# Kernel optimization log

Hardware: AMD Instinct MI355X
Metric: run time of the kernel (lower is better)

## Reference

```python
import jax, jax.numpy as jnp
import numpy as np

B, S, D, H = 2, 2048, 2048, 16
HD = D // H  # 128


def _rope_tables(seq_len, head_dim, base=10000.0):
    inv_freq = 1.0 / (base ** (np.arange(0, head_dim, 2, dtype=np.float32) / head_dim))
    t = np.arange(seq_len, dtype=np.float32)
    freqs = np.outer(t, inv_freq)  # [S, HD/2]
    return jnp.asarray(np.cos(freqs)), jnp.asarray(np.sin(freqs))


def setup_inputs() -> dict:
    key = jax.random.key(0)
    ks = jax.random.split(key, 5)
    std = 0.02
    inp = {
        "x": jax.random.normal(ks[0], (B, S, D), jnp.float32),
        "wq": jax.random.normal(ks[1], (D, D), jnp.float32) * std,
        "bq": jnp.zeros((D,), jnp.float32),
        "wk": jax.random.normal(ks[2], (D, D), jnp.float32) * std,
        "bk": jnp.zeros((D,), jnp.float32),
        "wv": jax.random.normal(ks[3], (D, D), jnp.float32) * std,
        "bv": jnp.zeros((D,), jnp.float32),
        "wo": jax.random.normal(ks[4], (D, D), jnp.float32) * std,
        "bo": jnp.zeros((D,), jnp.float32),
    }
    cos, sin = _rope_tables(S, HD)
    inp["freqs_cos"], inp["freqs_sin"] = cos, sin
    return inp


def _apply_rope(t, cos, sin):
    # t: [B,S,H,HD]; cos/sin: [S,HD/2] -> broadcast [1,S,1,HD/2]
    tp = t.reshape(*t.shape[:-1], HD // 2, 2)
    t1, t2 = tp[..., 0], tp[..., 1]
    c = cos[None, :, None, :]
    s = sin[None, :, None, :]
    out = jnp.stack([t1 * c - t2 * s, t1 * s + t2 * c], axis=-1)
    return out.reshape(t.shape)


def reference(x, wq, bq, wk, bk, wv, bv, wo, bo, freqs_cos, freqs_sin):
    b, s, d = x.shape
    q = (x @ wq.T + bq).reshape(b, s, H, HD)
    k = (x @ wk.T + bk).reshape(b, s, H, HD)
    v = (x @ wv.T + bv).reshape(b, s, H, HD)
    q = _apply_rope(q, freqs_cos, freqs_sin)
    k = _apply_rope(k, freqs_cos, freqs_sin)
    # causal SDPA: scores [B,H,S,S]
    scale = 1.0 / jnp.sqrt(jnp.asarray(HD, x.dtype))
    scores = jnp.einsum("bqhd,bkhd->bhqk", q, k) * scale
    causal = jnp.tril(jnp.ones((s, s), bool))
    scores = jnp.where(causal[None, None], scores, jnp.asarray(-1e30, scores.dtype))
    attn = jax.nn.softmax(scores.astype(jnp.float32), axis=-1).astype(x.dtype)
    out = jnp.einsum("bhqk,bkhd->bqhd", attn, v).reshape(b, s, d)
    return out @ wo.T + bo
```

## Files before the change

### kernel.cpp

```cpp
#include <hip/hip_runtime.h>


typedef __attribute__((ext_vector_type(8))) short short8;
typedef __attribute__((ext_vector_type(4))) float f32x4;
typedef __attribute__((ext_vector_type(16))) float f32x16;
typedef __attribute__((ext_vector_type(2))) unsigned short u16x2;
typedef __attribute__((ext_vector_type(4))) unsigned short u16x4;
typedef __attribute__((ext_vector_type(8))) unsigned short u16x8;

constexpr int Bc = 2, Sc = 2048, Dc = 2048, Hc = 16, HDc = 128;
constexpr int Mc = Bc * Sc;
constexpr int Nc = Dc, Kc = Dc;
constexpr int NT = Kc / 64;
constexpr float QSCL = 0.08838834764831845f * 1.4426950408889634f;

__device__ __forceinline__ unsigned short f2bf(float f) {
    union { float f; unsigned u; } x; x.f = f;
    unsigned r = x.u + 0x7FFFu + ((x.u >> 16) & 1u);
    return (unsigned short)(r >> 16);
}
__device__ __forceinline__ float bf2f(unsigned short u) {
    union { float f; unsigned u; } x; x.u = (unsigned)u << 16; return x.f;
}

__device__ __forceinline__ void g2lds16(const void* g, void* l) {
    __builtin_amdgcn_global_load_lds(
        (const __attribute__((address_space(1))) void*)g,
        (__attribute__((address_space(3))) void*)l, 16, 0, 0);
}

__device__ __forceinline__ void cvt_body(const float* __restrict__ in,
                                         unsigned short* __restrict__ out, int i) {
    f32x4 a = *((const f32x4*)in + (size_t)i * 2);
    f32x4 b = *((const f32x4*)in + (size_t)i * 2 + 1);
    u16x8 o;
    o[0] = f2bf(a[0]); o[1] = f2bf(a[1]); o[2] = f2bf(a[2]); o[3] = f2bf(a[3]);
    o[4] = f2bf(b[0]); o[5] = f2bf(b[1]); o[6] = f2bf(b[2]); o[7] = f2bf(b[3]);
    *((u16x8*)out + i) = o;
}

__global__ __launch_bounds__(256) void cvt_f32_bf16(
    const float* __restrict__ in, unsigned short* __restrict__ out, int n8) {
    int i = blockIdx.x * 256 + threadIdx.x;
    if (i >= n8) return;
    cvt_body(in, out, i);
}

__global__ __launch_bounds__(256) void cvt_all(
    const float* __restrict__ x,  unsigned short* __restrict__ xo,
    const float* __restrict__ w0, unsigned short* __restrict__ o0,
    const float* __restrict__ w1, unsigned short* __restrict__ o1,
    const float* __restrict__ w2, unsigned short* __restrict__ o2,
    const float* __restrict__ w3, unsigned short* __restrict__ o3) {
    int bid = blockIdx.x;
    const float* in; unsigned short* out;
    if (bid < 4096) { in = x; out = xo; }
    else {
        int r = bid - 4096, which = r >> 11;
        bid = r & 2047;
        if (which == 0)      { in = w0; out = o0; }
        else if (which == 1) { in = w1; out = o1; }
        else if (which == 2) { in = w2; out = o2; }
        else                 { in = w3; out = o3; }
    }
    cvt_body(in, out, bid * 256 + threadIdx.x);
}

#define G9_STAGE_A(tt, rr, ii) {                                               \
    int s_ = (ii) * 512 + tid, row_ = s_ >> 3, c_ = s_ & 7;                    \
    g2lds16(A + (size_t)(m0 + row_) * Kc + (tt) * 64 + ((c_ ^ (row_ & 7)) << 3), \
            &As[rr][(size_t)((ii) * 512 + (w << 6)) * 8]); }
#define G9_STAGE_B(tt, rr, ii) {                                               \
    int s_ = (ii) * 512 + tid, row_ = s_ >> 3, c_ = s_ & 7;                    \
    g2lds16(W + (size_t)(n0 + row_) * Kc + (tt) * 64 + ((c_ ^ (row_ & 7)) << 3), \
            &Bs[rr][(size_t)((ii) * 512 + (w << 6)) * 8]); }
#define G9_RD(rr, kk) { _Pragma("unroll")                                      \
    for (int i = 0; i < 4; ++i) {                                              \
        af[i] = *(const short8*)((const char*)As[rr] + offA[kk][i]);           \
        bf[i] = *(const short8*)((const char*)Bs[rr] + offB[kk][i]); } }
#define G9_MFMA16 { _Pragma("unroll")                                          \
    for (int i = 0; i < 4; ++i)                                                \
        _Pragma("unroll")                                                      \
        for (int j = 0; j < 4; ++j)                                            \
            acc[i][j] = __builtin_amdgcn_mfma_f32_16x16x32_bf16(af[i], bf[j], acc[i][j], 0, 0, 0); }
#define G9_SYNC1 __builtin_amdgcn_s_barrier();                                 \
    asm volatile("s_waitcnt lgkmcnt(0)" ::: "memory");                         \
    __builtin_amdgcn_s_setprio(1);
#define G9_SYNC2 __builtin_amdgcn_s_setprio(0); __builtin_amdgcn_s_barrier();

template <int KIND>
__global__ __launch_bounds__(512, 2) void gemm9(
    const unsigned short* __restrict__ A, const unsigned short* __restrict__ W,
    const float* __restrict__ bq, const float* __restrict__ bk,
    const float* __restrict__ bv, const float* __restrict__ rc,
    const float* __restrict__ rs, void* __restrict__ oq,
    unsigned short* __restrict__ ok, unsigned short* __restrict__ ov) {
    __shared__ __align__(16) unsigned short As[3][256 * 64];
    __shared__ __align__(16) unsigned short Bs[3][128 * 64];
    const int tid = threadIdx.x;
    const int w = tid >> 6, l = tid & 63;
    const int wm = w >> 1, wn = w & 1;
    const int lrow = l & 15, lhi = l >> 4;
    const int m0 = blockIdx.y * 256, n0 = blockIdx.x * 128;

    int offA[2][4], offB[2][4];
#pragma unroll
    for (int kk = 0; kk < 2; ++kk)
#pragma unroll
        for (int i = 0; i < 4; ++i) {
            int ra = wm * 64 + i * 16 + lrow;
            offA[kk][i] = (ra * 64 + (((kk * 4 + lhi) ^ (ra & 7)) << 3)) * 2;
            int rb = wn * 64 + i * 16 + lrow;
            offB[kk][i] = (rb * 64 + (((kk * 4 + lhi) ^ (rb & 7)) << 3)) * 2;
        }

    f32x4 acc[4][4];
#pragma unroll
    for (int i = 0; i < 4; ++i)
#pragma unroll
        for (int j = 0; j < 4; ++j) acc[i][j] = (f32x4){0.f, 0.f, 0.f, 0.f};

#pragma unroll
    for (int ii = 0; ii < 4; ++ii) G9_STAGE_A(0, 0, ii);
    G9_STAGE_B(0, 0, 0); G9_STAGE_B(0, 0, 1);
#pragma unroll
    for (int ii = 0; ii < 4; ++ii) G9_STAGE_A(1, 1, ii);
    G9_STAGE_B(1, 1, 0); G9_STAGE_B(1, 1, 1);
    asm volatile("s_waitcnt vmcnt(6)" ::: "memory");
    __builtin_amdgcn_s_barrier();

    short8 af[4], bf[4];
    for (int t = 0; t < NT; ++t) {
        const int r = t % 3, rn = (t + 2) % 3;
        const bool st = (t + 2) < NT;
        G9_RD(r, 0);
        if (st) { G9_STAGE_A(t + 2, rn, 0); G9_STAGE_A(t + 2, rn, 1); G9_STAGE_A(t + 2, rn, 2); }
        G9_SYNC1; G9_MFMA16; G9_SYNC2;
        G9_RD(r, 1);
        if (st) {
            G9_STAGE_A(t + 2, rn, 3); G9_STAGE_B(t + 2, rn, 0); G9_STAGE_B(t + 2, rn, 1);
            asm volatile("s_waitcnt vmcnt(6)" ::: "memory");
        } else {
            asm volatile("s_waitcnt vmcnt(0)" ::: "memory");
        }
        G9_SYNC1; G9_MFMA16; G9_SYNC2;
    }

    const int mode = (KIND == 1) ? 3 : (n0 >> 11);
    const float* bias = (KIND == 1) ? bq : (mode == 0 ? bq : mode == 1 ? bk : bv);
#pragma unroll
    for (int i = 0; i < 4; ++i) {
#pragma unroll
        for (int j = 0; j < 4; ++j) {
            int gm0 = m0 + wm * 64 + i * 16 + lhi * 4;
            int gn  = n0 + wn * 64 + j * 16 + lrow;
            int gnl = gn & (Dc - 1);
            float bvv = bias[gnl];
            if (mode == 0 || mode == 1) {
                unsigned short* o = (unsigned short*)(mode == 0 ? oq : (void*)ok);
                int fi = (gn & (HDc - 1)) >> 1;
#pragma unroll
                for (int rr = 0; rr < 4; ++rr) {
                    int gm = gm0 + rr;
                    float v = acc[i][j][rr] + bvv;
                    float p = __shfl_xor(v, 1);
                    int pos = gm & (Sc - 1);
                    float cz = rc[pos * (HDc / 2) + fi];
                    float sz = rs[pos * (HDc / 2) + fi];
                    float ovv = (gn & 1) ? (p * sz + v * cz) : (v * cz - p * sz);
                    if (mode == 0) ovv *= QSCL;
                    o[(size_t)gm * Dc + gnl] = f2bf(ovv);
                }
            } else if (mode == 2) {
                int b = gm0 >> 11, sb = gm0 & (Sc - 1);
                u16x4 pk;
#pragma unroll
                for (int rr = 0; rr < 4; ++rr) pk[rr] = f2bf(acc[i][j][rr] + bvv);
                *(u16x4*)&ov[((size_t)b * Dc + gnl) * Sc + sb] = pk;
            } else {
                float* o = (float*)oq;
#pragma unroll
                for (int rr = 0; rr < 4; ++rr)
                    o[(size_t)(gm0 + rr) * Nc + gn] = acc[i][j][rr] + bvv;
            }
        }
    }
}

template <int MODE>
__global__ __launch_bounds__(256) void gemm_nt(
    const unsigned short* __restrict__ A, const unsigned short* __restrict__ W,
    const float* __restrict__ bias, const float* __restrict__ rc,
    const float* __restrict__ rs, void* __restrict__ outp) {
    __shared__ __align__(16) unsigned short As[128 * 64];
    __shared__ __align__(16) unsigned short Bs[128 * 64];
    const int tid = threadIdx.x;
    const int w = tid >> 6, l = tid & 63;
    const int wm = w >> 1, wn = w & 1;
    const int lrow = l & 15, lhi = l >> 4;
    const int m0 = blockIdx.y * 128, n0 = blockIdx.x * 128;

    f32x4 acc[4][4];
#pragma unroll
    for (int i = 0; i < 4; ++i)
#pragma unroll
        for (int j = 0; j < 4; ++j) acc[i][j] = (f32x4){0.f, 0.f, 0.f, 0.f};

    for (int k0 = 0; k0 < Kc; k0 += 64) {
        __syncthreads();
#pragma unroll
        for (int i = 0; i < 4; ++i) {
            int s = i * 256 + tid;
            int row = s >> 3, c = s & 7;
            int cg = (c ^ (row & 7)) * 8;
            g2lds16(A + (size_t)(m0 + row) * Kc + k0 + cg,
                    &As[(size_t)(i * 256 + (w << 6)) * 8]);
            g2lds16(W + (size_t)(n0 + row) * Kc + k0 + cg,
                    &Bs[(size_t)(i * 256 + (w << 6)) * 8]);
        }
        __syncthreads();
#pragma unroll
        for (int kk = 0; kk < 2; ++kk) {
            short8 af[4], bf[4];
#pragma unroll
            for (int i = 0; i < 4; ++i) {
                int ra = wm * 64 + i * 16 + lrow;
                af[i] = *(const short8*)&As[ra * 64 + (((kk * 4 + lhi) ^ (ra & 7)) << 3)];
                int rb = wn * 64 + i * 16 + lrow;
                bf[i] = *(const short8*)&Bs[rb * 64 + (((kk * 4 + lhi) ^ (rb & 7)) << 3)];
            }
#pragma unroll
            for (int i = 0; i < 4; ++i)
#pragma unroll
                for (int j = 0; j < 4; ++j)
                    acc[i][j] = __builtin_amdgcn_mfma_f32_16x16x32_bf16(
                        af[i], bf[j], acc[i][j], 0, 0, 0);
        }
    }

#pragma unroll
    for (int i = 0; i < 4; ++i) {
#pragma unroll
        for (int j = 0; j < 4; ++j) {
            int gm0 = m0 + wm * 64 + i * 16 + lhi * 4;
            int gn  = n0 + wn * 64 + j * 16 + lrow;
            float bv = bias[gn];
            if (MODE == 0 || MODE == 1) {
                unsigned short* o = (unsigned short*)outp;
                int fi = (gn & (HDc - 1)) >> 1;
#pragma unroll
                for (int r = 0; r < 4; ++r) {
                    int gm = gm0 + r;
                    float v = acc[i][j][r] + bv;
                    float p = __shfl_xor(v, 1);
                    int pos = gm & (Sc - 1);
                    float cz = rc[pos * (HDc / 2) + fi];
                    float sz = rs[pos * (HDc / 2) + fi];
                    float ov = (gn & 1) ? (p * sz + v * cz) : (v * cz - p * sz);
                    if (MODE == 0) ov *= QSCL;
                    o[(size_t)gm * Nc + gn] = f2bf(ov);
                }
            } else if (MODE == 2) {
                unsigned short* o = (unsigned short*)outp;
                int b = gm0 >> 11, sb = gm0 & (Sc - 1);
                u16x4 pk;
#pragma unroll
                for (int r = 0; r < 4; ++r) pk[r] = f2bf(acc[i][j][r] + bv);
                *(u16x4*)&o[((size_t)b * Dc + gn) * Sc + sb] = pk;
            } else {
                float* o = (float*)outp;
#pragma unroll
                for (int r = 0; r < 4; ++r)
                    o[(size_t)(gm0 + r) * Nc + gn] = acc[i][j][r] + bv;
            }
        }
    }
}

#define ATTN_STAGE(tt, kd, vd) {                                               \
    const unsigned short* Kt = Kbase + (size_t)(tt) * 64 * Dc;                 \
    const unsigned short* Vp = Vbase + (tt) * 64;                              \
    _Pragma("unroll")                                                          \
    for (int i_ = 0; i_ < 4; ++i_) {                                           \
        int p_ = i_ * 256 + tid;                                               \
        int rK = p_ >> 4, sK = p_ & 15;                                        \
        g2lds16(Kt + (size_t)rK * Dc + ((sK ^ (rK & 15)) << 3),                \
                (kd) + (i_ * 256 + (w << 6)) * 8);                             \
        int rV = p_ >> 3, sV = p_ & 7;                                         \
        g2lds16(Vp + (size_t)rV * Sc + ((sV ^ (rV & 7)) << 3),                 \
                (vd) + (i_ * 256 + (w << 6)) * 8);                             \
    } }

#define ATTN_PVSTEP(PC, HB, KS) {                                              \
    int X0, X1, Y0, Y1;                                                        \
    asm("v_cvt_pk_bf16_f32 %0, %1, %2" : "=v"(X0) : "v"(PC[HB+0]), "v"(PC[HB+1])); \
    asm("v_cvt_pk_bf16_f32 %0, %1, %2" : "=v"(X1) : "v"(PC[HB+2]), "v"(PC[HB+3])); \
    asm("v_cvt_pk_bf16_f32 %0, %1, %2" : "=v"(Y0) : "v"(PC[HB+4]), "v"(PC[HB+5])); \
    asm("v_cvt_pk_bf16_f32 %0, %1, %2" : "=v"(Y1) : "v"(PC[HB+6]), "v"(PC[HB+7])); \
    asm("v_permlane32_swap_b32 %0, %1" : "+v"(X0), "+v"(Y0));                  \
    asm("v_permlane32_swap_b32 %0, %1" : "+v"(X1), "+v"(Y1));                  \
    union { int i[4]; short8 s; } pf_;                                         \
    pf_.i[0] = X0; pf_.i[1] = X1; pf_.i[2] = Y0; pf_.i[3] = Y1;                \
    _Pragma("unroll")                                                          \
    for (int dc_ = 0; dc_ < 4; ++dc_) {                                        \
        int rr = 32 * dc_ + ql;                                                \
        short8 vf = *(const short8*)&Vbuf[rr * 64 + (((2*(KS)+Hh) ^ (rr & 7)) << 3)]; \
        accv[dc_] = __builtin_amdgcn_mfma_f32_32x32x16_bf16(vf, pf_.s, accv[dc_], 0, 0, 0); \
    } }

#define ATTN_TILE_BODY(Kbuf, Vbuf, kb0)                                        \
    {                                                                          \
        f32x16 a0 = (f32x16)(0.f), a1 = (f32x16)(0.f);                         \
        __builtin_amdgcn_s_setprio(1);                                         \
        _Pragma("unroll")                                                      \
        for (int dc = 0; dc < 8; ++dc) {                                       \
            int r0 = ql, r1 = 32 + ql, sl = dc * 2 + Hh;                       \
            short8 k0 = *(const short8*)&Kbuf[r0 * 128 + ((sl ^ (r0 & 15)) << 3)]; \
            short8 k1 = *(const short8*)&Kbuf[r1 * 128 + ((sl ^ (r1 & 15)) << 3)]; \
            a0 = __builtin_amdgcn_mfma_f32_32x32x16_bf16(k0, qf[dc], a0, 0, 0, 0); \
            a1 = __builtin_amdgcn_mfma_f32_32x32x16_bf16(k1, qf[dc], a1, 0, 0, 0); \
        }                                                                      \
        __builtin_amdgcn_s_setprio(0);                                         \
        if ((kb0) >= 2 * qt * 64) {                                            \
            _Pragma("unroll")                                                  \
            for (int r = 0; r < 16; ++r) {                                     \
                int kl = (r & 3) + 8 * (r >> 2) + 4 * Hh;                      \
                if ((kb0) + kl > qg)      a0[r] = -3.0e38f;                    \
                if ((kb0) + 32 + kl > qg) a1[r] = -3.0e38f;                    \
            }                                                                  \
        }                                                                      \
        float m8[8];                                                           \
        _Pragma("unroll")                                                      \
        for (int r = 0; r < 8; ++r)                                            \
            m8[r] = fmaxf(fmaxf(a0[r], a0[r + 8]), fmaxf(a1[r], a1[r + 8]));   \
        float m4a = fmaxf(m8[0], m8[1]), m4b = fmaxf(m8[2], m8[3]);            \
        float m4c = fmaxf(m8[4], m8[5]), m4d = fmaxf(m8[6], m8[7]);            \
        float pm = fmaxf(fmaxf(m4a, m4b), fmaxf(m4c, m4d));                    \
        pm = fmaxf(pm, __shfl_xor(pm, 32));                                    \
        if (!__all(pm - mrun <= 8.0f)) {                                       \
            float mnew = fmaxf(mrun, pm);                                      \
            float fs = exp2f(mrun - mnew);                                     \
            mrun = mnew;                                                       \
            lrun *= fs;                                                        \
            _Pragma("unroll")                                                  \
            for (int dc = 0; dc < 4; ++dc)                                     \
                _Pragma("unroll")                                              \
                for (int r = 0; r < 16; ++r) accv[dc][r] *= fs;                \
        }                                                                      \
        float p0[16], p1[16];                                                  \
        _Pragma("unroll")                                                      \
        for (int r = 0; r < 16; ++r) p0[r] = exp2f(a0[r] - mrun);              \
        _Pragma("unroll")                                                      \
        for (int r = 0; r < 16; ++r) p1[r] = exp2f(a1[r] - mrun);              \
        float s8[8];                                                           \
        _Pragma("unroll")                                                      \
        for (int r = 0; r < 8; ++r)                                            \
            s8[r] = (p0[r] + p0[r + 8]) + (p1[r] + p1[r + 8]);                 \
        float s4a = s8[0] + s8[1], s4b = s8[2] + s8[3];                        \
        float s4c = s8[4] + s8[5], s4d = s8[6] + s8[7];                        \
        float ps = (s4a + s4b) + (s4c + s4d);                                  \
        lrun += ps + __shfl_xor(ps, 32);                                       \
        __builtin_amdgcn_s_setprio(1);                                         \
        ATTN_PVSTEP(p0, 0, 0); ATTN_PVSTEP(p0, 8, 1);                          \
        ATTN_PVSTEP(p1, 0, 2); ATTN_PVSTEP(p1, 8, 3);                          \
        __builtin_amdgcn_s_setprio(0);                                         \
    }

__global__ __launch_bounds__(256, 2) void attn_part(
    const unsigned short* __restrict__ Q, const unsigned short* __restrict__ Kb,
    const unsigned short* __restrict__ Vt, unsigned short* __restrict__ O,
    unsigned short* __restrict__ pacc, float* __restrict__ pml) {
    __shared__ __align__(16) unsigned short Ks[2][64 * 128];
    __shared__ __align__(16) unsigned short Vs[2][128 * 64];
    const int tid = threadIdx.x;
    const int w = tid >> 6, l = tid & 63;
    const int ql = l & 31, Hh = l >> 5;
    const int bh = blockIdx.x;
    const int slot = blockIdx.y;
    int qt, part, np;
    if (slot < 16) { qt = 15 - (slot >> 1); part = slot & 1; np = 2; }
    else           { qt = 23 - slot;        part = 0;        np = 1; }
    const int nt   = 2 * qt + 2;
    const int tbeg = part ? (qt + 1) : 0;
    const int tend = (np == 2 && part == 0) ? (qt + 1) : nt;
    const int b = bh >> 4, h = bh & 15;

    const unsigned short* Kbase = Kb + ((size_t)b * Sc) * Dc + h * HDc;
    const unsigned short* Vbase = Vt + ((size_t)b * Dc + h * HDc) * Sc;

    const int qw0 = qt * 128 + w * 32;
    const int qg = qw0 + ql;

    short8 qf[8];
    {
        const unsigned short* qp = Q + ((size_t)(b * Sc + qg)) * Dc + h * HDc;
#pragma unroll
        for (int dc = 0; dc < 8; ++dc)
            qf[dc] = *(const short8*)(qp + dc * 16 + Hh * 8);
    }
    f32x16 accv[4];
#pragma unroll
    for (int i = 0; i < 4; ++i) accv[i] = (f32x16)(0.f);
    float mrun = -3.0e38f, lrun = 0.f;

    ATTN_STAGE(tbeg, Ks[0], Vs[0]);
    for (int t = tbeg; t < tend; ++t) {
        const int cur = (t - tbeg) & 1;
        if (t + 1 < tend) {
            ATTN_STAGE(t + 1, Ks[cur ^ 1], Vs[cur ^ 1]);
            asm volatile("s_waitcnt vmcnt(8)" ::: "memory");
        } else {
            asm volatile("s_waitcnt vmcnt(0)" ::: "memory");
        }
        __builtin_amdgcn_s_barrier();

        const unsigned short* Kbuf = Ks[cur];
        const unsigned short* Vbuf = Vs[cur];
        const int kb0 = t * 64;
        if (kb0 <= qw0 + 31) ATTN_TILE_BODY(Kbuf, Vbuf, kb0);
        __builtin_amdgcn_s_barrier();
    }

    if (np == 1) {
        float inv = 1.f / lrun;
        unsigned short* Op = O + ((size_t)(b * Sc + qg)) * Dc + h * HDc;
#pragma unroll
        for (int dc = 0; dc < 4; ++dc)
#pragma unroll
            for (int rg = 0; rg < 4; ++rg) {
                int d0 = 32 * dc + 8 * rg + 4 * Hh;
                u16x4 pk;
#pragma unroll
                for (int j = 0; j < 4; ++j) pk[j] = f2bf(accv[dc][rg * 4 + j] * inv);
                *(u16x4*)(Op + d0) = pk;
            }
    } else {
        const int jslot = ((bh << 3) + (qt - 8)) * 2 + part;
        unsigned short* pa = pacc + (size_t)jslot * (128 * 128) + (w * 32 + ql) * 128;
#pragma unroll
        for (int dc = 0; dc < 4; ++dc)
#pragma unroll
            for (int rg = 0; rg < 4; ++rg) {
                u16x4 pk;
#pragma unroll
                for (int j = 0; j < 4; ++j) pk[j] = f2bf(accv[dc][rg * 4 + j]);
                *(u16x4*)&pa[32 * dc + 8 * rg + 4 * Hh] = pk;
            }
        if (Hh == 0) {
            float* pm2 = pml + (size_t)jslot * 256 + (w * 32 + ql) * 2;
            pm2[0] = mrun; pm2[1] = lrun;
        }
    }
}

__global__ __launch_bounds__(256) void attn_combine(
    const unsigned short* __restrict__ pacc, const float* __restrict__ pml,
    unsigned short* __restrict__ O) {
    const int w = threadIdx.x >> 6, l = threadIdx.x & 63;
    const int idx = blockIdx.x * 4 + w;
    const int jp = idx >> 7, row = idx & 127;
    const int bh = jp >> 3, qt = (jp & 7) + 8;
    const int b = bh >> 4, h = bh & 15;
    const unsigned short* a0 = pacc + ((size_t)jp * 2) * (128 * 128) + row * 128;
    const unsigned short* a1 = a0 + 128 * 128;
    const float* ml0 = pml + ((size_t)jp * 2) * 256 + row * 2;
    const float* ml1 = ml0 + 256;
    float m0 = ml0[0], l0 = ml0[1], m1 = ml1[0], l1 = ml1[1];
    float M = fmaxf(m0, m1);
    float w0 = exp2f(m0 - M), w1 = exp2f(m1 - M);
    float inv = 1.f / (l0 * w0 + l1 * w1);
    int d = l * 2;
    u16x2 v0 = *(const u16x2*)&a0[d];
    u16x2 v1 = *(const u16x2*)&a1[d];
    u16x2 pk;
    pk[0] = f2bf((bf2f(v0[0]) * w0 + bf2f(v1[0]) * w1) * inv);
    pk[1] = f2bf((bf2f(v0[1]) * w0 + bf2f(v1[1]) * w1) * inv);
    int qrow = qt * 128 + row;
    *(u16x2*)(O + ((size_t)(b * Sc + qrow)) * Dc + h * HDc + d) = pk;
}

__global__ __launch_bounds__(256, 2) void attn_fwd5(
    const unsigned short* __restrict__ Q, const unsigned short* __restrict__ Kb,
    const unsigned short* __restrict__ Vt, unsigned short* __restrict__ O) {
    __shared__ __align__(16) unsigned short Ks[2][64 * 128];
    __shared__ __align__(16) unsigned short Vs[2][128 * 64];
    const int tid = threadIdx.x;
    const int w = tid >> 6, l = tid & 63;
    const int ql = l & 31, Hh = l >> 5;
    const int bh = blockIdx.x;
    const int y = blockIdx.y;
    const int qt = (y < 8) ? y : (23 - y);
    const int b = bh >> 4, h = bh & 15;

    const unsigned short* Kbase = Kb + ((size_t)b * Sc) * Dc + h * HDc;
    const unsigned short* Vbase = Vt + ((size_t)b * Dc + h * HDc) * Sc;

    const int qw0 = qt * 128 + w * 32;
    const int qg = qw0 + ql;

    short8 qf[8];
    {
        const unsigned short* qp = Q + ((size_t)(b * Sc + qg)) * Dc + h * HDc;
#pragma unroll
        for (int dc = 0; dc < 8; ++dc)
            qf[dc] = *(const short8*)(qp + dc * 16 + Hh * 8);
    }
    f32x16 accv[4];
#pragma unroll
    for (int i = 0; i < 4; ++i) accv[i] = (f32x16)(0.f);
    float mrun = -3.0e38f, lrun = 0.f;
    const int nt = 2 * qt + 2;

    ATTN_STAGE(0, Ks[0], Vs[0]);
    for (int t = 0; t < nt; ++t) {
        if (t + 1 < nt) {
            ATTN_STAGE(t + 1, Ks[(t + 1) & 1], Vs[(t + 1) & 1]);
            asm volatile("s_waitcnt vmcnt(8)" ::: "memory");
        } else {
            asm volatile("s_waitcnt vmcnt(0)" ::: "memory");
        }
        __builtin_amdgcn_s_barrier();

        const unsigned short* Kbuf = Ks[t & 1];
        const unsigned short* Vbuf = Vs[t & 1];
        const int kb0 = t * 64;
        if (kb0 <= qw0 + 31) ATTN_TILE_BODY(Kbuf, Vbuf, kb0);
        __builtin_amdgcn_s_barrier();
    }
    float inv = 1.f / lrun;
    unsigned short* Op = O + ((size_t)(b * Sc + qg)) * Dc + h * HDc;
#pragma unroll
    for (int dc = 0; dc < 4; ++dc)
#pragma unroll
        for (int rg = 0; rg < 4; ++rg) {
            int d0 = 32 * dc + 8 * rg + 4 * Hh;
            u16x4 pk;
#pragma unroll
            for (int j = 0; j < 4; ++j) pk[j] = f2bf(accv[dc][rg * 4 + j] * inv);
            *(u16x4*)(Op + d0) = pk;
        }
}

extern "C" void kernel_launch(void* const* d_in, const int* in_sizes, int n_in,
                              void* d_out, int out_size, void* d_ws, size_t ws_size,
                              hipStream_t stream) {
    const float* x  = (const float*)d_in[0];
    const float* wq = (const float*)d_in[1];
    const float* bq = (const float*)d_in[2];
    const float* wk = (const float*)d_in[3];
    const float* bk = (const float*)d_in[4];
    const float* wv = (const float*)d_in[5];
    const float* bv = (const float*)d_in[6];
    const float* wo = (const float*)d_in[7];
    const float* bo = (const float*)d_in[8];
    const float* rc = (const float*)d_in[9];
    const float* rs = (const float*)d_in[10];

    const size_t NE = (size_t)Mc * Dc;
    const size_t NW = (size_t)Dc * Dc;

    unsigned short* xb = (unsigned short*)d_ws;
    unsigned short* qb = xb + NE;
    unsigned short* kb = qb + NE;
    unsigned short* vt = kb + NE;
    unsigned short* wb = vt + NE;

    const int ne8 = (int)(NE / 8), nw8 = (int)(NW / 8);
    dim3 tb(256);
    const bool big_ws = ws_size >= (4 * NE + 4 * NW) * sizeof(unsigned short);

    if (big_ws) {
        unsigned short* wqb = wb;
        unsigned short* wkb = wb + NW;
        unsigned short* wvb = wb + 2 * NW;
        unsigned short* wob = wb + 3 * NW;
        unsigned short* pacc = wb;
        float* pml = (float*)(wb + 2 * NW);
        cvt_all<<<dim3(4096 + 4 * 2048), tb, 0, stream>>>(
            x, xb, wq, wqb, wk, wkb, wv, wvb, wo, wob);
        gemm9<0><<<dim3(Nc * 3 / 128, Mc / 256), dim3(512), 0, stream>>>(
            xb, wb, bq, bk, bv, rc, rs, qb, kb, vt);
        attn_part<<<dim3(Bc * Hc, 24), tb, 0, stream>>>(qb, kb, vt, xb, pacc, pml);
        attn_combine<<<dim3(32 * 8 * 128 / 4), tb, 0, stream>>>(pacc, pml, xb);
        gemm9<1><<<dim3(Nc / 128, Mc / 256), dim3(512), 0, stream>>>(
            xb, wob, bo, nullptr, nullptr, rc, rs, d_out, nullptr, nullptr);
    } else {
        dim3 gg(Nc / 128, Mc / 128);
        cvt_f32_bf16<<<dim3(ne8 / 256), tb, 0, stream>>>(x, xb, ne8);
        cvt_f32_bf16<<<dim3(nw8 / 256), tb, 0, stream>>>(wq, wb, nw8);
        gemm_nt<0><<<gg, tb, 0, stream>>>(xb, wb, bq, rc, rs, qb);
        cvt_f32_bf16<<<dim3(nw8 / 256), tb, 0, stream>>>(wk, wb, nw8);
        gemm_nt<1><<<gg, tb, 0, stream>>>(xb, wb, bk, rc, rs, kb);
        cvt_f32_bf16<<<dim3(nw8 / 256), tb, 0, stream>>>(wv, wb, nw8);
        gemm_nt<2><<<gg, tb, 0, stream>>>(xb, wb, bv, rc, rs, vt);
        attn_fwd5<<<dim3(Bc * Hc, 16), tb, 0, stream>>>(qb, kb, vt, xb);
        cvt_f32_bf16<<<dim3(nw8 / 256), tb, 0, stream>>>(wo, wb, nw8);
        gemm_nt<3><<<gg, tb, 0, stream>>>(xb, wb, bo, rc, rs, d_out);
    }
}
```

Before: 248.8 us.

## Single-buffer V in attn_part and split load schedule to raise occupancy

The attn_part kernel keeps only one V tile in LDS instead of two. V for the current tile is now loaded at the start of each iteration and overlaps with the QK^T and softmax work, with a second wait and barrier before the PV matmul. This cuts LDS per block from 64KB to 48KB, so launch_bounds can rise from 2 to 3 blocks per CU. The cost is an extra barrier per tile, exposed V load latency, and tighter register limits. attn_fwd5 is unchanged apart from renaming its buffer.

```diff
diff --git a/kernel.cpp b/kernel.cpp
--- a/kernel.cpp
+++ b/kernel.cpp
@@ -277,21 +277,27 @@
     }
 }
 
-#define ATTN_STAGE(tt, kd, vd) {                                               \
+#define ATTN_STAGE_K(tt, kd) {                                                 \
     const unsigned short* Kt = Kbase + (size_t)(tt) * 64 * Dc;                 \
-    const unsigned short* Vp = Vbase + (tt) * 64;                              \
     _Pragma("unroll")                                                          \
     for (int i_ = 0; i_ < 4; ++i_) {                                           \
         int p_ = i_ * 256 + tid;                                               \
         int rK = p_ >> 4, sK = p_ & 15;                                        \
         g2lds16(Kt + (size_t)rK * Dc + ((sK ^ (rK & 15)) << 3),                \
                 (kd) + (i_ * 256 + (w << 6)) * 8);                             \
+    } }
+#define ATTN_STAGE_V(tt, vd) {                                                 \
+    const unsigned short* Vp = Vbase + (tt) * 64;                              \
+    _Pragma("unroll")                                                          \
+    for (int i_ = 0; i_ < 4; ++i_) {                                           \
+        int p_ = i_ * 256 + tid;                                               \
         int rV = p_ >> 3, sV = p_ & 7;                                         \
         g2lds16(Vp + (size_t)rV * Sc + ((sV ^ (rV & 7)) << 3),                 \
                 (vd) + (i_ * 256 + (w << 6)) * 8);                             \
     } }
-
-#define ATTN_PVSTEP(PC, HB, KS) {                                              \
+#define ATTN_STAGE(tt, kd, vd) { ATTN_STAGE_K(tt, kd); ATTN_STAGE_V(tt, vd); }
+
+#define ATTN_PVSTEP(PC, HB, KS, Vbuf) {                                        \
     int X0, X1, Y0, Y1;                                                        \
     asm("v_cvt_pk_bf16_f32 %0, %1, %2" : "=v"(X0) : "v"(PC[HB+0]), "v"(PC[HB+1])); \
     asm("v_cvt_pk_bf16_f32 %0, %1, %2" : "=v"(X1) : "v"(PC[HB+2]), "v"(PC[HB+3])); \
@@ -304,19 +310,19 @@
     _Pragma("unroll")                                                          \
     for (int dc_ = 0; dc_ < 4; ++dc_) {                                        \
         int rr = 32 * dc_ + ql;                                                \
-        short8 vf = *(const short8*)&Vbuf[rr * 64 + (((2*(KS)+Hh) ^ (rr & 7)) << 3)]; \
+        short8 vf = *(const short8*)&(Vbuf)[rr * 64 + (((2*(KS)+Hh) ^ (rr & 7)) << 3)]; \
         accv[dc_] = __builtin_amdgcn_mfma_f32_32x32x16_bf16(vf, pf_.s, accv[dc_], 0, 0, 0); \
     } }
 
-#define ATTN_TILE_BODY(Kbuf, Vbuf, kb0)                                        \
+#define ATTN_QKT_SM(Kbuf, kb0)                                                 \
     {                                                                          \
         f32x16 a0 = (f32x16)(0.f), a1 = (f32x16)(0.f);                         \
         __builtin_amdgcn_s_setprio(1);                                         \
         _Pragma("unroll")                                                      \
         for (int dc = 0; dc < 8; ++dc) {                                       \
             int r0 = ql, r1 = 32 + ql, sl = dc * 2 + Hh;                       \
-            short8 k0 = *(const short8*)&Kbuf[r0 * 128 + ((sl ^ (r0 & 15)) << 3)]; \
-            short8 k1 = *(const short8*)&Kbuf[r1 * 128 + ((sl ^ (r1 & 15)) << 3)]; \
+            short8 k0 = *(const short8*)&(Kbuf)[r0 * 128 + ((sl ^ (r0 & 15)) << 3)]; \
+            short8 k1 = *(const short8*)&(Kbuf)[r1 * 128 + ((sl ^ (r1 & 15)) << 3)]; \
             a0 = __builtin_amdgcn_mfma_f32_32x32x16_bf16(k0, qf[dc], a0, 0, 0, 0); \
             a1 = __builtin_amdgcn_mfma_f32_32x32x16_bf16(k1, qf[dc], a1, 0, 0, 0); \
         }                                                                      \
@@ -347,7 +353,6 @@
                 _Pragma("unroll")                                              \
                 for (int r = 0; r < 16; ++r) accv[dc][r] *= fs;                \
         }                                                                      \
-        float p0[16], p1[16];                                                  \
         _Pragma("unroll")                                                      \
         for (int r = 0; r < 16; ++r) p0[r] = exp2f(a0[r] - mrun);              \
         _Pragma("unroll")                                                      \
@@ -360,18 +365,27 @@
         float s4c = s8[4] + s8[5], s4d = s8[6] + s8[7];                        \
         float ps = (s4a + s4b) + (s4c + s4d);                                  \
         lrun += ps + __shfl_xor(ps, 32);                                       \
+    }
+
+#define ATTN_PV(Vbuf) {                                                        \
         __builtin_amdgcn_s_setprio(1);                                         \
-        ATTN_PVSTEP(p0, 0, 0); ATTN_PVSTEP(p0, 8, 1);                          \
-        ATTN_PVSTEP(p1, 0, 2); ATTN_PVSTEP(p1, 8, 3);                          \
+        ATTN_PVSTEP(p0, 0, 0, Vbuf); ATTN_PVSTEP(p0, 8, 1, Vbuf);              \
+        ATTN_PVSTEP(p1, 0, 2, Vbuf); ATTN_PVSTEP(p1, 8, 3, Vbuf);              \
         __builtin_amdgcn_s_setprio(0);                                         \
     }
 
-__global__ __launch_bounds__(256, 2) void attn_part(
+#define ATTN_TILE_BODY(Kbuf, Vbuf, kb0) {                                      \
+        float p0[16], p1[16];                                                  \
+        ATTN_QKT_SM(Kbuf, kb0);                                                \
+        ATTN_PV(Vbuf);                                                         \
+    }
+
+__global__ __launch_bounds__(256, 3) void attn_part(
     const unsigned short* __restrict__ Q, const unsigned short* __restrict__ Kb,
     const unsigned short* __restrict__ Vt, unsigned short* __restrict__ O,
     unsigned short* __restrict__ pacc, float* __restrict__ pml) {
     __shared__ __align__(16) unsigned short Ks[2][64 * 128];
-    __shared__ __align__(16) unsigned short Vs[2][128 * 64];
+    __shared__ __align__(16) unsigned short Vs[128 * 64];
     const int tid = threadIdx.x;
     const int w = tid >> 6, l = tid & 63;
     const int ql = l & 31, Hh = l >> 5;
@@ -403,21 +417,29 @@
     for (int i = 0; i < 4; ++i) accv[i] = (f32x16)(0.f);
     float mrun = -3.0e38f, lrun = 0.f;
 
-    ATTN_STAGE(tbeg, Ks[0], Vs[0]);
+    ATTN_STAGE_K(tbeg, Ks[0]);
     for (int t = tbeg; t < tend; ++t) {
         const int cur = (t - tbeg) & 1;
-        if (t + 1 < tend) {
-            ATTN_STAGE(t + 1, Ks[cur ^ 1], Vs[cur ^ 1]);
+        ATTN_STAGE_V(t, Vs);
+        const bool sk = (t + 1 < tend);
+        if (sk) {
+            ATTN_STAGE_K(t + 1, Ks[cur ^ 1]);
             asm volatile("s_waitcnt vmcnt(8)" ::: "memory");
         } else {
-            asm volatile("s_waitcnt vmcnt(0)" ::: "memory");
+            asm volatile("s_waitcnt vmcnt(4)" ::: "memory");
         }
         __builtin_amdgcn_s_barrier();
 
         const unsigned short* Kbuf = Ks[cur];
-        const unsigned short* Vbuf = Vs[cur];
         const int kb0 = t * 64;
-        if (kb0 <= qw0 + 31) ATTN_TILE_BODY(Kbuf, Vbuf, kb0);
+        const bool act = (kb0 <= qw0 + 31);
+        float p0[16], p1[16];
+        if (act) ATTN_QKT_SM(Kbuf, kb0);
+
+        if (sk) asm volatile("s_waitcnt vmcnt(4)" ::: "memory");
+        else    asm volatile("s_waitcnt vmcnt(0)" ::: "memory");
+        __builtin_amdgcn_s_barrier();
+        if (act) ATTN_PV(Vs);
         __builtin_amdgcn_s_barrier();
     }
 
@@ -483,7 +505,7 @@
     const unsigned short* __restrict__ Q, const unsigned short* __restrict__ Kb,
     const unsigned short* __restrict__ Vt, unsigned short* __restrict__ O) {
     __shared__ __align__(16) unsigned short Ks[2][64 * 128];
-    __shared__ __align__(16) unsigned short Vs[2][128 * 64];
+    __shared__ __align__(16) unsigned short Vs2[2][128 * 64];
     const int tid = threadIdx.x;
     const int w = tid >> 6, l = tid & 63;
     const int ql = l & 31, Hh = l >> 5;
@@ -511,10 +533,10 @@
     float mrun = -3.0e38f, lrun = 0.f;
     const int nt = 2 * qt + 2;
 
-    ATTN_STAGE(0, Ks[0], Vs[0]);
+    ATTN_STAGE(0, Ks[0], Vs2[0]);
     for (int t = 0; t < nt; ++t) {
         if (t + 1 < nt) {
-            ATTN_STAGE(t + 1, Ks[(t + 1) & 1], Vs[(t + 1) & 1]);
+            ATTN_STAGE(t + 1, Ks[(t + 1) & 1], Vs2[(t + 1) & 1]);
             asm volatile("s_waitcnt vmcnt(8)" ::: "memory");
         } else {
             asm volatile("s_waitcnt vmcnt(0)" ::: "memory");
@@ -522,7 +544,7 @@
         __builtin_amdgcn_s_barrier();
 
         const unsigned short* Kbuf = Ks[t & 1];
-        const unsigned short* Vbuf = Vs[t & 1];
+        const unsigned short* Vbuf = Vs2[t & 1];
         const int kb0 = t * 64;
         if (kb0 <= qw0 + 31) ATTN_TILE_BODY(Kbuf, Vbuf, kb0);
         __builtin_amdgcn_s_barrier();
```

After: 260.7 us. 4.8% more time.
